# Optimization experiments

Measured on AMD Instinct MI355X. Metric: run time of the kernel, lower is better.

The kernel has to match this reference:

```python
import jax, jax.numpy as jnp
import numpy as np

N_RAYS = 32768
HID = 64
MARCH_ITERS = 64
EPS = 1e-4
NEAR = 0.0
FAR = 1.0
T_FAR = 1.0
TPUT_B = 64
JITTER = 1.0 / TPUT_B  # fixed stand-in for random.random() * (2 / batch_size)


def _init_linear(key, fan_in, fan_out):
    kw, kb = jax.random.split(key)
    lim = 1.0 / np.sqrt(fan_in)
    W = jax.random.uniform(kw, (fan_in, fan_out), jnp.float32, -lim, lim)
    b = jax.random.uniform(kb, (fan_out,), jnp.float32, -lim, lim)
    return W, b


def setup_inputs() -> dict:
    key = jax.random.key(0)
    ks = jax.random.split(key, 6)
    rays = jax.random.normal(ks[0], (N_RAYS, 6), jnp.float32)
    W0, b0 = _init_linear(ks[1], 3, HID)
    W1, b1 = _init_linear(ks[2], HID, HID)
    W2, b2 = _init_linear(ks[3], HID, 1)
    Wr0, br0 = _init_linear(ks[4], 6, HID)
    Wr1, br1 = _init_linear(ks[5], HID, 3)
    return dict(rays=rays, W0=W0, b0=b0, W1=W1, b1=b1, W2=W2, b2=b2,
                Wr0=Wr0, br0=br0, Wr1=Wr1, br1=br1)


def _sdf(p, W0, b0, W1, b1, W2, b2):
    # p: [N, 3] -> signed distance [N, 1]
    h = jax.nn.relu(p @ W0 + b0)
    h = jax.nn.relu(h @ W1 + b1)
    return h @ W2 + b2


def _refl(p, d, Wr0, br0, Wr1, br1):
    # p, d: [N, 3] -> RGB [N, 3]
    h = jax.nn.relu(jnp.concatenate([p, d], axis=-1) @ Wr0 + br0)
    return jax.nn.sigmoid(h @ Wr1 + br1)


def reference(rays, W0, b0, W1, b1, W2, b2, Wr0, br0, Wr1, br1):
    r_o, r_d = rays[..., :3], rays[..., 3:]
    sdf = lambda p: _sdf(p, W0, b0, W1, b1, W2, b2)

    # --- sphere march (64 fixed iterations; early-exit break is a no-op
    # once all rays hit, since hit rays stop updating) ---
    hits0 = jnp.zeros(r_o.shape[:-1] + (1,), jnp.bool_)
    dist0 = jnp.full(r_o.shape[:-1] + (1,), NEAR, jnp.float32)

    def march(carry, _):
        hits, cd = carry
        d = sdf(r_o + r_d * cd)  # [N, 1]
        hits = hits | ((d < EPS) & (cd >= NEAR) & (cd <= FAR))
        cd = jnp.where(~hits, cd + d, cd)
        return (hits, cd), None

    (hit, t), _ = jax.lax.scan(march, (hits0, dist0), None, length=MARCH_ITERS)
    pts = r_o + r_d * t

    rgb = _refl(pts, r_d, Wr0, br0, Wr1, br1)
    rgb = jnp.where(hit, rgb, 0.0)  # out[~hit] = 0

    # --- throughput (index search under no_grad in the original) ---
    max_t = T_FAR + JITTER
    step = max_t / TPUT_B
    sg = jax.lax.stop_gradient
    sdf_ng = lambda p: _sdf(p, sg(W0), sg(b0), sg(W1), sg(b1), sg(W2), sg(b2))
    r_o_ng, r_d_ng = sg(r_o), sg(r_d)

    curr_min0 = sdf_ng(r_o_ng)[..., 0]          # [N]
    idxs0 = jnp.zeros_like(curr_min0, jnp.int32)

    def tloop(carry, i):
        cm, idxs = carry
        t_i = step * (i + 1).astype(jnp.float32)
        sd = sdf_ng(r_o_ng + t_i * r_d_ng)[..., 0]
        idxs = jnp.where(sd < cm, i + 1, idxs)
        return (jnp.minimum(cm, sd), idxs), None

    (_, idxs), _ = jax.lax.scan(tloop, (curr_min0, idxs0),
                                jnp.arange(TPUT_B, dtype=jnp.int32))

    best_pos = r_o + idxs[..., None].astype(jnp.float32) * step * r_d  # [N, 3]
    tput = sdf(best_pos)  # [N, 1], differentiable (outside no_grad in torch)

    return jnp.concatenate([rgb, tput], axis=-1)  # [N, 4]
```

## Files before the change

### kernel.cpp

```cpp
#include <hip/hip_runtime.h>
#include <math.h>

#define NRAYS        32768
#define MARCH_ITERS  64
#define EPS_         1e-4f
#define STEP_        ((1.0f + 1.0f/64.0f) / 64.0f)

typedef __attribute__((ext_vector_type(8)))  short    short8;
typedef __attribute__((ext_vector_type(4)))  float    float4v;
typedef __attribute__((ext_vector_type(2)))  float    float2v;
typedef __attribute__((ext_vector_type(4)))  unsigned uint4v;

__device__ __forceinline__ short8 mk_frag(unsigned p0, unsigned p1,
                                          unsigned p2, unsigned p3) {
    uint4v v = {p0, p1, p2, p3};
    return __builtin_bit_cast(short8, v);
}

__device__ __forceinline__ unsigned packbf(unsigned a, unsigned b) {
    return __builtin_amdgcn_perm(b, a, 0x07060302u);
}

struct Split2 { unsigned h, r; };
__device__ __forceinline__ Split2 split2(float x) {
    unsigned xu = __float_as_uint(x);
    float xh = __uint_as_float(xu & 0xFFFF0000u);
    float rr = x - xh;
    return { xu, __float_as_uint(rr) };
}

__device__ __forceinline__ float2v fma2(float2v a, float2v b, float2v c) {
    return __builtin_elementwise_fma(a, b, c);
}

__global__ __launch_bounds__(64)
__attribute__((amdgpu_waves_per_eu(2, 8)))
void sdf_w10_k(
    const float* __restrict__ rays,
    const float* __restrict__ W0,  const float* __restrict__ b0,
    const float* __restrict__ W1,  const float* __restrict__ b1,
    const float* __restrict__ W2,  const float* __restrict__ b2,
    const float* __restrict__ Wr0, const float* __restrict__ br0,
    const float* __restrict__ Wr1, const float* __restrict__ br1,
    float* __restrict__ out)
{
    const int lane = threadIdx.x;
    const int kind = blockIdx.x & 1;
    const int quad = lane >> 4;
    const int m    = lane & 15;
    const int rayBase = (blockIdx.x >> 1) * 16;

    const float* rp = rays + (rayBase + m) * 6;
    const float ox = rp[0], oy = rp[1], oz = rp[2];
    const float dx = rp[3], dy = rp[4], dz = rp[5];

    float2v a2[4][2], s2[4][2];
    #pragma unroll
    for (int t = 0; t < 4; ++t)
        #pragma unroll
        for (int p = 0; p < 2; ++p) {
            float av[2], sv[2];
            #pragma unroll
            for (int e = 0; e < 2; ++e) {
                int j = 32 * (t >> 1) + 8 * quad + 4 * (t & 1) + (2 * p + e);
                float w0c = W0[j], w1c = W0[64 + j], w2c = W0[128 + j];
                av[e] = fmaf(ox, w0c, fmaf(oy, w1c, fmaf(oz, w2c, b0[j])));
                sv[e] = fmaf(dx, w0c, fmaf(dy, w1c, dz * w2c));
            }
            a2[t][p] = (float2v){av[0], av[1]};
            s2[t][p] = (float2v){sv[0], sv[1]};
        }

    float4v b1v[4];
    float2v w2a[4], w2b[4];
    #pragma unroll
    for (int t = 0; t < 4; ++t) {
        int base = 16 * t + 4 * quad;
        b1v[t] = (float4v){b1[base], b1[base + 1], b1[base + 2], b1[base + 3]};
        w2a[t] = (float2v){W2[base], W2[base + 1]};
        w2b[t] = (float2v){W2[base + 2], W2[base + 3]};
    }
    const float b2s = b2[0];

    auto front = [&](float cv, short8* BH, short8* BM) {
        const float2v c2 = {cv, cv};
        unsigned PH[4][2], PM[4][2];
        #pragma unroll
        for (int t = 0; t < 4; ++t) {
            float2v v01 = fma2(c2, s2[t][0], a2[t][0]);
            float2v v23 = fma2(c2, s2[t][1], a2[t][1]);
            float v0 = fmaxf(v01.x, 0.f), v1 = fmaxf(v01.y, 0.f);
            float v2 = fmaxf(v23.x, 0.f), v3 = fmaxf(v23.y, 0.f);
            unsigned u0 = __float_as_uint(v0), u1 = __float_as_uint(v1);
            unsigned u2 = __float_as_uint(v2), u3 = __float_as_uint(v3);
            PH[t][0] = packbf(u0, u1); PH[t][1] = packbf(u2, u3);
            float2v h01 = {__uint_as_float(u0 & 0xFFFF0000u),
                           __uint_as_float(u1 & 0xFFFF0000u)};
            float2v h23 = {__uint_as_float(u2 & 0xFFFF0000u),
                           __uint_as_float(u3 & 0xFFFF0000u)};
            float2v r01 = (float2v){v0, v1} - h01;
            float2v r23 = (float2v){v2, v3} - h23;
            PM[t][0] = packbf(__float_as_uint(r01.x), __float_as_uint(r01.y));
            PM[t][1] = packbf(__float_as_uint(r23.x), __float_as_uint(r23.y));
        }
        #pragma unroll
        for (int h = 0; h < 2; ++h) {
            BH[h] = mk_frag(PH[2 * h][0], PH[2 * h][1],
                            PH[2 * h + 1][0], PH[2 * h + 1][1]);
            BM[h] = mk_frag(PM[2 * h][0], PM[2 * h][1],
                            PM[2 * h + 1][0], PM[2 * h + 1][1]);
        }
    };

    auto l3 = [&](const float4v* C2) -> float {
        float2v q01 = {0.f, 0.f}, q23 = {0.f, 0.f};
        #pragma unroll
        for (int t = 0; t < 4; ++t) {
            float2v rel01 = {fmaxf(C2[t][0], 0.f), fmaxf(C2[t][1], 0.f)};
            float2v rel23 = {fmaxf(C2[t][2], 0.f), fmaxf(C2[t][3], 0.f)};
            q01 = fma2(rel01, w2a[t], q01);
            q23 = fma2(rel23, w2b[t], q23);
        }
        float part = (q01.x + q01.y) + (q23.x + q23.y);
        part += __shfl_xor(part, 16, 64);
        part += __shfl_xor(part, 32, 64);
        return b2s + part;
    };

    if (kind == 0) {
        short8 A2h[2][4], A2m[2][4];
        #pragma unroll
        for (int h = 0; h < 2; ++h)
            #pragma unroll
            for (int t = 0; t < 4; ++t) {
                unsigned pm[4], ph[4];
                #pragma unroll
                for (int jp = 0; jp < 4; ++jp) {
                    int k0 = 32 * h + quad * 8 + 2 * jp;
                    int j2 = 16 * t + m;
                    Split2 a = split2(W1[k0 * 64 + j2]);
                    Split2 b = split2(W1[(k0 + 1) * 64 + j2]);
                    pm[jp] = packbf(a.r, b.r);
                    ph[jp] = packbf(a.h, b.h);
                }
                A2m[h][t] = mk_frag(pm[0], pm[1], pm[2], pm[3]);
                A2h[h][t] = mk_frag(ph[0], ph[1], ph[2], ph[3]);
            }

        bool  hit = false;
        float cd  = 0.f;
        #pragma unroll 1
        for (int it = 0; it < MARCH_ITERS; ++it) {
            if (__all(hit)) break;
            short8 BH[2], BM[2];
            front(cd, BH, BM);
            float4v C2[4];
            #pragma unroll
            for (int t = 0; t < 4; ++t)
                C2[t] = __builtin_amdgcn_mfma_f32_16x16x32_bf16(
                    A2m[0][t], BH[0], b1v[t], 0, 0, 0);
            #pragma unroll
            for (int t = 0; t < 4; ++t)
                C2[t] = __builtin_amdgcn_mfma_f32_16x16x32_bf16(
                    A2m[1][t], BH[1], C2[t], 0, 0, 0);
            #pragma unroll
            for (int h = 0; h < 2; ++h)
                #pragma unroll
                for (int t = 0; t < 4; ++t)
                    C2[t] = __builtin_amdgcn_mfma_f32_16x16x32_bf16(
                        A2h[h][t], BM[h], C2[t], 0, 0, 0);
            #pragma unroll
            for (int h = 0; h < 2; ++h)
                #pragma unroll
                for (int t = 0; t < 4; ++t)
                    C2[t] = __builtin_amdgcn_mfma_f32_16x16x32_bf16(
                        A2h[h][t], BH[h], C2[t], 0, 0, 0);
            float dm = l3(C2);
            bool c = (dm < EPS_) && (cd >= 0.f) && (cd <= 1.f);
            hit = hit || c;
            if (!hit) cd += dm;
        }

        const float px = fmaf(dx, cd, ox), py = fmaf(dy, cd, oy), pz = fmaf(dz, cd, oz);
        float r0 = 0.f, r1 = 0.f, r2 = 0.f;
        #pragma unroll 4
        for (int jj = 0; jj < 16; ++jj) {
            int j = quad * 16 + jj;
            float a = fmaf(px, Wr0[j],
                      fmaf(py, Wr0[64 + j],
                      fmaf(pz, Wr0[128 + j],
                      fmaf(dx, Wr0[192 + j],
                      fmaf(dy, Wr0[256 + j],
                      fmaf(dz, Wr0[320 + j], br0[j]))))));
            a = fmaxf(a, 0.f);
            r0 = fmaf(a, Wr1[j * 3 + 0], r0);
            r1 = fmaf(a, Wr1[j * 3 + 1], r1);
            r2 = fmaf(a, Wr1[j * 3 + 2], r2);
        }
        r0 += __shfl_xor(r0, 16, 64); r0 += __shfl_xor(r0, 32, 64);
        r1 += __shfl_xor(r1, 16, 64); r1 += __shfl_xor(r1, 32, 64);
        r2 += __shfl_xor(r2, 16, 64); r2 += __shfl_xor(r2, 32, 64);
        r0 = 1.f / (1.f + expf(-(r0 + br1[0])));
        r1 = 1.f / (1.f + expf(-(r1 + br1[1])));
        r2 = 1.f / (1.f + expf(-(r2 + br1[2])));
        if (!hit) { r0 = 0.f; r1 = 0.f; r2 = 0.f; }
        if (lane < 16) {
            float* op = out + (rayBase + lane) * 4;
            op[0] = r0; op[1] = r1; op[2] = r2;
        }
    } else {
        short8 A2h[2][4];
        #pragma unroll
        for (int h = 0; h < 2; ++h)
            #pragma unroll
            for (int t = 0; t < 4; ++t) {
                unsigned ph[4];
                #pragma unroll
                for (int jp = 0; jp < 4; ++jp) {
                    int k0 = 32 * h + quad * 8 + 2 * jp;
                    int j2 = 16 * t + m;
                    ph[jp] = packbf(__float_as_uint(W1[k0 * 64 + j2]),
                                    __float_as_uint(W1[(k0 + 1) * 64 + j2]));
                }
                A2h[h][t] = mk_frag(ph[0], ph[1], ph[2], ph[3]);
            }

        float cm = 3.4e38f;
        #pragma unroll 1
        for (int i = 0; i <= 64; ++i) {
            float ti = STEP_ * (float)i;
            short8 BH[2], BM[2];
            front(ti, BH, BM);
            float4v C2[4];
            #pragma unroll
            for (int t = 0; t < 4; ++t)
                C2[t] = __builtin_amdgcn_mfma_f32_16x16x32_bf16(
                    A2h[0][t], BM[0], b1v[t], 0, 0, 0);
            #pragma unroll
            for (int t = 0; t < 4; ++t)
                C2[t] = __builtin_amdgcn_mfma_f32_16x16x32_bf16(
                    A2h[1][t], BM[1], C2[t], 0, 0, 0);
            #pragma unroll
            for (int h = 0; h < 2; ++h)
                #pragma unroll
                for (int t = 0; t < 4; ++t)
                    C2[t] = __builtin_amdgcn_mfma_f32_16x16x32_bf16(
                        A2h[h][t], BH[h], C2[t], 0, 0, 0);
            float dt = l3(C2);
            cm = fminf(cm, dt);
        }
        if (lane < 16)
            out[(rayBase + lane) * 4 + 3] = cm;
    }
}

extern "C" void kernel_launch(void* const* d_in, const int* in_sizes, int n_in,
                              void* d_out, int out_size, void* d_ws, size_t ws_size,
                              hipStream_t stream) {
    const float* rays = (const float*)d_in[0];
    const float* W0   = (const float*)d_in[1];
    const float* b0   = (const float*)d_in[2];
    const float* W1   = (const float*)d_in[3];
    const float* b1   = (const float*)d_in[4];
    const float* W2   = (const float*)d_in[5];
    const float* b2   = (const float*)d_in[6];
    const float* Wr0  = (const float*)d_in[7];
    const float* br0  = (const float*)d_in[8];
    const float* Wr1  = (const float*)d_in[9];
    const float* br1  = (const float*)d_in[10];
    float* out = (float*)d_out;

    hipLaunchKernelGGL(sdf_w10_k, dim3((NRAYS / 16) * 2), dim3(64), 0, stream,
                       rays, W0, b0, W1, b1, W2, b2, Wr0, br0, Wr1, br1, out);
}
```

Baseline: 182.4 us.

## Fuse march and throughput waves into one interleaved per-ray loop

Instead of launching separate blocks for the sphere march and the throughput search, each wave now does both. The two MFMA chains are interleaved in one loop while marching is active, then the loop finishes the remaining throughput samples alone. This halves the grid, shares setup work (ray loads, W1 fragment preparation), exposes two independent MFMA dependency chains for ILP, and merges the output into one float4 store. In exchange it raises register pressure, since both A2m and A2h plus two accumulator sets are live, and removes the parallelism of separate waves, which could lower occupancy.

New measurement: 167.9 us. 1.09x faster.

```diff
diff --git a/kernel.cpp b/kernel.cpp
--- a/kernel.cpp
+++ b/kernel.cpp
@@ -35,7 +35,7 @@
 
 __global__ __launch_bounds__(64)
 __attribute__((amdgpu_waves_per_eu(2, 8)))
-void sdf_w10_k(
+void sdf_w11_k(
     const float* __restrict__ rays,
     const float* __restrict__ W0,  const float* __restrict__ b0,
     const float* __restrict__ W1,  const float* __restrict__ b1,
@@ -45,10 +45,9 @@
     float* __restrict__ out)
 {
     const int lane = threadIdx.x;
-    const int kind = blockIdx.x & 1;
     const int quad = lane >> 4;
     const int m    = lane & 15;
-    const int rayBase = (blockIdx.x >> 1) * 16;
+    const int rayBase = blockIdx.x * 16;
 
     const float* rp = rays + (rayBase + m) * 6;
     const float ox = rp[0], oy = rp[1], oz = rp[2];
@@ -81,6 +80,25 @@
         w2b[t] = (float2v){W2[base + 2], W2[base + 3]};
     }
     const float b2s = b2[0];
+
+    short8 A2h[2][4], A2m[2][4];
+    #pragma unroll
+    for (int h = 0; h < 2; ++h)
+        #pragma unroll
+        for (int t = 0; t < 4; ++t) {
+            unsigned pm[4], ph[4];
+            #pragma unroll
+            for (int jp = 0; jp < 4; ++jp) {
+                int k0 = 32 * h + quad * 8 + 2 * jp;
+                int j2 = 16 * t + m;
+                Split2 a = split2(W1[k0 * 64 + j2]);
+                Split2 b = split2(W1[(k0 + 1) * 64 + j2]);
+                pm[jp] = packbf(a.r, b.r);
+                ph[jp] = packbf(a.h, b.h);
+            }
+            A2m[h][t] = mk_frag(pm[0], pm[1], pm[2], pm[3]);
+            A2h[h][t] = mk_frag(ph[0], ph[1], ph[2], ph[3]);
+        }
 
     auto front = [&](float cv, short8* BH, short8* BM) {
         const float2v c2 = {cv, cv};
@@ -127,130 +145,101 @@
         return b2s + part;
     };
 
-    if (kind == 0) {
-        short8 A2h[2][4], A2m[2][4];
+    auto tputC2 = [&](const short8* BHt, const short8* BMt, float4v* C2t) {
+        #pragma unroll
+        for (int t = 0; t < 4; ++t)
+            C2t[t] = __builtin_amdgcn_mfma_f32_16x16x32_bf16(
+                A2h[0][t], BMt[0], b1v[t], 0, 0, 0);
+        #pragma unroll
+        for (int t = 0; t < 4; ++t)
+            C2t[t] = __builtin_amdgcn_mfma_f32_16x16x32_bf16(
+                A2h[1][t], BMt[1], C2t[t], 0, 0, 0);
         #pragma unroll
         for (int h = 0; h < 2; ++h)
             #pragma unroll
-            for (int t = 0; t < 4; ++t) {
-                unsigned pm[4], ph[4];
-                #pragma unroll
-                for (int jp = 0; jp < 4; ++jp) {
-                    int k0 = 32 * h + quad * 8 + 2 * jp;
-                    int j2 = 16 * t + m;
-                    Split2 a = split2(W1[k0 * 64 + j2]);
-                    Split2 b = split2(W1[(k0 + 1) * 64 + j2]);
-                    pm[jp] = packbf(a.r, b.r);
-                    ph[jp] = packbf(a.h, b.h);
-                }
-                A2m[h][t] = mk_frag(pm[0], pm[1], pm[2], pm[3]);
-                A2h[h][t] = mk_frag(ph[0], ph[1], ph[2], ph[3]);
-            }
-
-        bool  hit = false;
-        float cd  = 0.f;
-        #pragma unroll 1
-        for (int it = 0; it < MARCH_ITERS; ++it) {
-            if (__all(hit)) break;
-            short8 BH[2], BM[2];
-            front(cd, BH, BM);
-            float4v C2[4];
-            #pragma unroll
             for (int t = 0; t < 4; ++t)
-                C2[t] = __builtin_amdgcn_mfma_f32_16x16x32_bf16(
-                    A2m[0][t], BH[0], b1v[t], 0, 0, 0);
+                C2t[t] = __builtin_amdgcn_mfma_f32_16x16x32_bf16(
+                    A2h[h][t], BHt[h], C2t[t], 0, 0, 0);
+    };
+
+    bool  hit = false;
+    float cd  = 0.f;
+    float cm  = 3.4e38f;
+    int   i   = 0;
+
+    #pragma unroll 1
+    for (; i <= 64; ++i) {
+        if (i >= MARCH_ITERS || __all(hit)) break;
+        float ti = STEP_ * (float)i;
+        short8 BHt[2], BMt[2];
+        front(ti, BHt, BMt);
+        short8 BHm[2], BMm[2];
+        front(cd, BHm, BMm);
+        float4v C2m[4], C2t[4];
+        #pragma unroll
+        for (int t = 0; t < 4; ++t)
+            C2m[t] = __builtin_amdgcn_mfma_f32_16x16x32_bf16(
+                A2m[0][t], BHm[0], b1v[t], 0, 0, 0);
+        #pragma unroll
+        for (int t = 0; t < 4; ++t)
+            C2m[t] = __builtin_amdgcn_mfma_f32_16x16x32_bf16(
+                A2m[1][t], BHm[1], C2m[t], 0, 0, 0);
+        #pragma unroll
+        for (int h = 0; h < 2; ++h)
             #pragma unroll
             for (int t = 0; t < 4; ++t)
-                C2[t] = __builtin_amdgcn_mfma_f32_16x16x32_bf16(
-                    A2m[1][t], BH[1], C2[t], 0, 0, 0);
-            #pragma unroll
-            for (int h = 0; h < 2; ++h)
-                #pragma unroll
-                for (int t = 0; t < 4; ++t)
-                    C2[t] = __builtin_amdgcn_mfma_f32_16x16x32_bf16(
-                        A2h[h][t], BM[h], C2[t], 0, 0, 0);
-            #pragma unroll
-            for (int h = 0; h < 2; ++h)
-                #pragma unroll
-                for (int t = 0; t < 4; ++t)
-                    C2[t] = __builtin_amdgcn_mfma_f32_16x16x32_bf16(
-                        A2h[h][t], BH[h], C2[t], 0, 0, 0);
-            float dm = l3(C2);
-            bool c = (dm < EPS_) && (cd >= 0.f) && (cd <= 1.f);
-            hit = hit || c;
-            if (!hit) cd += dm;
-        }
-
-        const float px = fmaf(dx, cd, ox), py = fmaf(dy, cd, oy), pz = fmaf(dz, cd, oz);
-        float r0 = 0.f, r1 = 0.f, r2 = 0.f;
-        #pragma unroll 4
-        for (int jj = 0; jj < 16; ++jj) {
-            int j = quad * 16 + jj;
-            float a = fmaf(px, Wr0[j],
-                      fmaf(py, Wr0[64 + j],
-                      fmaf(pz, Wr0[128 + j],
-                      fmaf(dx, Wr0[192 + j],
-                      fmaf(dy, Wr0[256 + j],
-                      fmaf(dz, Wr0[320 + j], br0[j]))))));
-            a = fmaxf(a, 0.f);
-            r0 = fmaf(a, Wr1[j * 3 + 0], r0);
-            r1 = fmaf(a, Wr1[j * 3 + 1], r1);
-            r2 = fmaf(a, Wr1[j * 3 + 2], r2);
-        }
-        r0 += __shfl_xor(r0, 16, 64); r0 += __shfl_xor(r0, 32, 64);
-        r1 += __shfl_xor(r1, 16, 64); r1 += __shfl_xor(r1, 32, 64);
-        r2 += __shfl_xor(r2, 16, 64); r2 += __shfl_xor(r2, 32, 64);
-        r0 = 1.f / (1.f + expf(-(r0 + br1[0])));
-        r1 = 1.f / (1.f + expf(-(r1 + br1[1])));
-        r2 = 1.f / (1.f + expf(-(r2 + br1[2])));
-        if (!hit) { r0 = 0.f; r1 = 0.f; r2 = 0.f; }
-        if (lane < 16) {
-            float* op = out + (rayBase + lane) * 4;
-            op[0] = r0; op[1] = r1; op[2] = r2;
-        }
-    } else {
-        short8 A2h[2][4];
+                C2m[t] = __builtin_amdgcn_mfma_f32_16x16x32_bf16(
+                    A2h[h][t], BMm[h], C2m[t], 0, 0, 0);
         #pragma unroll
         for (int h = 0; h < 2; ++h)
             #pragma unroll
-            for (int t = 0; t < 4; ++t) {
-                unsigned ph[4];
-                #pragma unroll
-                for (int jp = 0; jp < 4; ++jp) {
-                    int k0 = 32 * h + quad * 8 + 2 * jp;
-                    int j2 = 16 * t + m;
-                    ph[jp] = packbf(__float_as_uint(W1[k0 * 64 + j2]),
-                                    __float_as_uint(W1[(k0 + 1) * 64 + j2]));
-                }
-                A2h[h][t] = mk_frag(ph[0], ph[1], ph[2], ph[3]);
-            }
-
-        float cm = 3.4e38f;
-        #pragma unroll 1
-        for (int i = 0; i <= 64; ++i) {
-            float ti = STEP_ * (float)i;
-            short8 BH[2], BM[2];
-            front(ti, BH, BM);
-            float4v C2[4];
-            #pragma unroll
             for (int t = 0; t < 4; ++t)
-                C2[t] = __builtin_amdgcn_mfma_f32_16x16x32_bf16(
-                    A2h[0][t], BM[0], b1v[t], 0, 0, 0);
-            #pragma unroll
-            for (int t = 0; t < 4; ++t)
-                C2[t] = __builtin_amdgcn_mfma_f32_16x16x32_bf16(
-                    A2h[1][t], BM[1], C2[t], 0, 0, 0);
-            #pragma unroll
-            for (int h = 0; h < 2; ++h)
-                #pragma unroll
-                for (int t = 0; t < 4; ++t)
-                    C2[t] = __builtin_amdgcn_mfma_f32_16x16x32_bf16(
-                        A2h[h][t], BH[h], C2[t], 0, 0, 0);
-            float dt = l3(C2);
-            cm = fminf(cm, dt);
-        }
-        if (lane < 16)
-            out[(rayBase + lane) * 4 + 3] = cm;
+                C2m[t] = __builtin_amdgcn_mfma_f32_16x16x32_bf16(
+                    A2h[h][t], BHm[h], C2m[t], 0, 0, 0);
+        tputC2(BHt, BMt, C2t);
+        float dm = l3(C2m);
+        bool c = (dm < EPS_) && (cd >= 0.f) && (cd <= 1.f);
+        hit = hit || c;
+        if (!hit) cd += dm;
+        cm = fminf(cm, l3(C2t));
+    }
+
+    #pragma unroll 1
+    for (; i <= 64; ++i) {
+        float ti = STEP_ * (float)i;
+        short8 BHt[2], BMt[2];
+        front(ti, BHt, BMt);
+        float4v C2t[4];
+        tputC2(BHt, BMt, C2t);
+        cm = fminf(cm, l3(C2t));
+    }
+
+    const float px = fmaf(dx, cd, ox), py = fmaf(dy, cd, oy), pz = fmaf(dz, cd, oz);
+    float r0 = 0.f, r1 = 0.f, r2 = 0.f;
+    #pragma unroll 4
+    for (int jj = 0; jj < 16; ++jj) {
+        int j = quad * 16 + jj;
+        float a = fmaf(px, Wr0[j],
+                  fmaf(py, Wr0[64 + j],
+                  fmaf(pz, Wr0[128 + j],
+                  fmaf(dx, Wr0[192 + j],
+                  fmaf(dy, Wr0[256 + j],
+                  fmaf(dz, Wr0[320 + j], br0[j]))))));
+        a = fmaxf(a, 0.f);
+        r0 = fmaf(a, Wr1[j * 3 + 0], r0);
+        r1 = fmaf(a, Wr1[j * 3 + 1], r1);
+        r2 = fmaf(a, Wr1[j * 3 + 2], r2);
+    }
+    r0 += __shfl_xor(r0, 16, 64); r0 += __shfl_xor(r0, 32, 64);
+    r1 += __shfl_xor(r1, 16, 64); r1 += __shfl_xor(r1, 32, 64);
+    r2 += __shfl_xor(r2, 16, 64); r2 += __shfl_xor(r2, 32, 64);
+    r0 = 1.f / (1.f + expf(-(r0 + br1[0])));
+    r1 = 1.f / (1.f + expf(-(r1 + br1[1])));
+    r2 = 1.f / (1.f + expf(-(r2 + br1[2])));
+    if (!hit) { r0 = 0.f; r1 = 0.f; r2 = 0.f; }
+    if (lane < 16) {
+        float4v o4 = {r0, r1, r2, cm};
+        *reinterpret_cast<float4v*>(out + (rayBase + lane) * 4) = o4;
     }
 }
 
@@ -270,6 +259,6 @@
     const float* br1  = (const float*)d_in[10];
     float* out = (float*)d_out;
 
-    hipLaunchKernelGGL(sdf_w10_k, dim3((NRAYS / 16) * 2), dim3(64), 0, stream,
+    hipLaunchKernelGGL(sdf_w11_k, dim3(NRAYS / 16), dim3(64), 0, stream,
                        rays, W0, b0, W1, b1, W2, b2, Wr0, br0, Wr1, br1, out);
 }
```
